# Optimization experiments

Hardware: AMD Instinct MI355X
Metric: run time of the kernel (lower is better)

The kernel has to match this reference:

```python
import jax, jax.numpy as jnp
import numpy as np

B, L, H, C = 32, 2048, 512, 50
KERNEL = 3  # avgpool kernel, stride 1, pad 1, count_include_pad=False


def _avgpool3_no_pad_count(x):
    """AvgPool1d(kernel=3, stride=1, pad=1, count_include_pad=False) along last axis.
    x: (..., L). Zero-pad, sum 3-tap windows, divide by number of valid elements."""
    pad = [(0, 0)] * (x.ndim - 1) + [(1, 1)]
    xp = jnp.pad(x, pad)
    s = xp[..., :-2] + xp[..., 1:-1] + xp[..., 2:]
    ones = jnp.pad(jnp.ones_like(x), pad)
    cnt = ones[..., :-2] + ones[..., 1:-1] + ones[..., 2:]
    return s / cnt


def setup_inputs() -> dict:
    key = jax.random.key(0)
    k1, k2, k3, k4, k5, k6 = jax.random.split(key, 6)
    sent_keys = jax.random.normal(k1, (B, L, H), dtype=jnp.float32)
    sent_values = jax.random.normal(k2, (B, L, H), dtype=jnp.float32)
    sent_lens = jax.random.randint(k3, (B,), 1, L + 1).astype(jnp.int64)
    W1 = jax.random.normal(k4, (H, H), dtype=jnp.float32) * 0.02
    W2 = jax.random.normal(k5, (H, H), dtype=jnp.float32) * 0.02
    W3 = jax.random.normal(k6, (C, H), dtype=jnp.float32) * 0.02
    return {"sent_keys": sent_keys, "sent_values": sent_values,
            "sent_lens": sent_lens, "W1": W1, "W2": W2, "W3": W3}


def reference(sent_keys, sent_values, sent_lens, W1, W2, W3):
    # Tiny MLP scorer (dropout is identity in eval mode)
    p1 = jnp.tanh(jnp.einsum('blh,kh->blk', sent_keys, W1))   # (B,L,H)
    p2 = jnp.tanh(jnp.einsum('blh,kh->blk', p1, W2))          # (B,L,H)
    p3 = jnp.einsum('blh,ch->blc', p1 + p2, W3)               # (B,L,C)

    b, l, c = p3.shape
    # Fill padded positions with the score at the last valid position (index len-1)
    last_idx = (sent_lens - 1).astype(jnp.int32)[:, None, None]        # (B,1,1)
    last = jnp.take_along_axis(p3, jnp.broadcast_to(last_idx, (b, 1, c)), axis=1)  # (B,1,C)
    mask = (jnp.arange(l)[None, :] < sent_lens[:, None])[:, :, None]   # (B,L,1)
    kq = jnp.where(mask, p3, last)

    # Smooth along doc-position axis with avgpool(count_include_pad=False)
    smoothened_kq = _avgpool3_no_pad_count(kq.transpose(0, 2, 1)).transpose(0, 2, 1)  # (B,L,C)

    # Softmax over classes, then zero out padded positions
    attention_values = jax.nn.softmax(smoothened_kq, axis=2)
    attention_values = jnp.where(mask, attention_values, 0.0)

    # (B,C,L) @ (B,L,H) -> (B,C,H)
    class_inputs = jnp.einsum('blc,blh->bch', attention_values, sent_values)
    return attention_values, class_inputs, smoothened_kq
```

## Files before the change

### kernel.cpp

```cpp
#include <hip/hip_runtime.h>
#include <cstdint>

#define Bc 32
#define Lc 2048
#define Hc 512
#define Cc 50
#define PCc 52
#define Mc (Bc*Lc)

typedef short s8v   __attribute__((ext_vector_type(8)));
typedef float f4v   __attribute__((ext_vector_type(4)));

__device__ inline unsigned short f2bf(float f) {
    unsigned int u = __float_as_uint(f);
    u += 0x7fffu + ((u >> 16) & 1u);
    return (unsigned short)(u >> 16);
}
__device__ inline float bf2f(unsigned short h) {
    return __uint_as_float(((unsigned int)h) << 16);
}
__device__ inline float fast_tanh(float x) {
    float e = __expf(2.0f * x);
    return 1.0f - 2.0f / (e + 1.0f);
}
__device__ inline void gl_lds16(const unsigned short* g, unsigned short* l) {
    __builtin_amdgcn_global_load_lds(
        (const __attribute__((address_space(1))) unsigned int*)g,
        (__attribute__((address_space(3))) unsigned int*)l, 16, 0, 0);
}

__global__ __launch_bounds__(256)
void f32_to_bf16_kernel(const float* __restrict__ in, unsigned short* __restrict__ out)
{
    size_t i = ((size_t)blockIdx.x * 256 + threadIdx.x) * 8;
    float4 a = *(const float4*)(in + i);
    float4 b = *(const float4*)(in + i + 4);
    s8v o;
    o[0]=f2bf(a.x); o[1]=f2bf(a.y); o[2]=f2bf(a.z); o[3]=f2bf(a.w);
    o[4]=f2bf(b.x); o[5]=f2bf(b.y); o[6]=f2bf(b.z); o[7]=f2bf(b.w);
    *(s8v*)(out + i) = o;
}

__global__ __launch_bounds__(256)
void convert_weights_kernel(const float* __restrict__ W1, const float* __restrict__ W2,
                            const float* __restrict__ W3,
                            unsigned short* __restrict__ W1b,
                            unsigned short* __restrict__ W2b,
                            unsigned short* __restrict__ W3b)
{
    int e = (blockIdx.x * 256 + threadIdx.x) * 8;
    if (e >= 524288) {
        int off = e - 524288;
        int row = off >> 9;
        s8v o;
        #pragma unroll
        for (int j = 0; j < 8; ++j)
            o[j] = (row < Cc) ? (short)f2bf(W3[off + j]) : (short)0;
        *(s8v*)(W3b + off) = o;
        return;
    }
    const float* src = (e < 262144) ? W1 : W2;
    unsigned short* dst = (e < 262144) ? W1b : W2b;
    int off = (e < 262144) ? e : e - 262144;
    float4 a = *(const float4*)(src + off);
    float4 b = *(const float4*)(src + off + 4);
    s8v o;
    o[0]=f2bf(a.x); o[1]=f2bf(a.y); o[2]=f2bf(a.z); o[3]=f2bf(a.w);
    o[4]=f2bf(b.x); o[5]=f2bf(b.y); o[6]=f2bf(b.z); o[7]=f2bf(b.w);
    *(s8v*)(dst + off) = o;
}

__global__ __launch_bounds__(256)
void transpose_v_kernel(const float* __restrict__ V, unsigned short* __restrict__ Vt)
{
    __shared__ float tile[64 * 65];
    const int l0 = blockIdx.x * 64;
    const int h0 = blockIdx.y * 64;
    const int b  = blockIdx.z;
    const int tid = threadIdx.x;
    const int li = tid >> 2;
    const int hq = (tid & 3) * 4;

    const float* src = V + ((size_t)(b * Lc + l0 + li)) * Hc + h0 + hq;
    #pragma unroll
    for (int j = 0; j < 4; ++j) {
        float4 v = *(const float4*)(src + 16 * j);
        float* d = &tile[li * 65 + hq + 16 * j];
        d[0] = v.x; d[1] = v.y; d[2] = v.z; d[3] = v.w;
    }
    __syncthreads();

    const int lane = tid & 63;
    const int w    = tid >> 6;
    #pragma unroll
    for (int i = 0; i < 16; ++i) {
        int hr = i * 4 + w;
        unsigned short* dst = Vt + ((size_t)(b * Hc + h0 + hr)) * Lc + l0 + lane;
        *dst = f2bf(tile[lane * 65 + hr]);
    }
}

__global__ __launch_bounds__(256)
void mfma_gemm512(const unsigned short* __restrict__ Ab,
                  const unsigned short* __restrict__ Wb,
                  unsigned short* __restrict__ Ob, int mode)
{
    __shared__ alignas(16) unsigned short As[128 * 32];
    __shared__ alignas(16) unsigned short Bs[128 * 32];
    const int tid = threadIdx.x;
    const int w = tid >> 6, l = tid & 63;
    const int j0 = blockIdx.x * 128;
    const int i0 = blockIdx.y * 128;

    const int sr  = w * 16 + (l >> 2);
    const int kg8 = (l & 3) * 8;
    const unsigned short* Ag0 = Ab + (size_t)(i0 + sr) * 512 + kg8;
    const unsigned short* Ag1 = Ag0 + (size_t)64 * 512;
    const unsigned short* Bg0 = Wb + (size_t)(j0 + sr) * 512 + kg8;
    const unsigned short* Bg1 = Bg0 + (size_t)64 * 512;
    unsigned short* Al0 = As + w * 512;
    unsigned short* Al1 = As + 2048 + w * 512;
    unsigned short* Bl0 = Bs + w * 512;
    unsigned short* Bl1 = Bs + 2048 + w * 512;

    const int wm = (w & 1) * 64, wn = (w >> 1) * 64;
    const int fr = l & 15;
    const int fq = (l >> 4) * 8;

    f4v acc[4][4];
    #pragma unroll
    for (int r = 0; r < 4; ++r)
        #pragma unroll
        for (int c = 0; c < 4; ++c) acc[r][c] = (f4v){0.f, 0.f, 0.f, 0.f};

    for (int k0 = 0; k0 < 512; k0 += 32) {
        gl_lds16(Ag0 + k0, Al0);
        gl_lds16(Ag1 + k0, Al1);
        gl_lds16(Bg0 + k0, Bl0);
        gl_lds16(Bg1 + k0, Bl1);
        __syncthreads();
        s8v af[4], bf[4];
        #pragma unroll
        for (int r = 0; r < 4; ++r)
            af[r] = *(const s8v*)&As[(wm + r * 16 + fr) * 32 + fq];
        #pragma unroll
        for (int c = 0; c < 4; ++c)
            bf[c] = *(const s8v*)&Bs[(wn + c * 16 + fr) * 32 + fq];
        #pragma unroll
        for (int r = 0; r < 4; ++r)
            #pragma unroll
            for (int c = 0; c < 4; ++c)
                acc[r][c] = __builtin_amdgcn_mfma_f32_16x16x32_bf16(
                    af[r], bf[c], acc[r][c], 0, 0, 0);
        __syncthreads();
    }

    #pragma unroll
    for (int r = 0; r < 4; ++r)
        #pragma unroll
        for (int v = 0; v < 4; ++v) {
            const int row = i0 + wm + r * 16 + (l >> 4) * 4 + v;
            #pragma unroll
            for (int c = 0; c < 4; ++c) {
                const int col = j0 + wn + c * 16 + fr;
                float x = fast_tanh(acc[r][c][v]);
                if (mode) x += bf2f(Ab[(size_t)row * 512 + col]);
                Ob[(size_t)row * 512 + col] = f2bf(x);
            }
        }
}

__global__ __launch_bounds__(256)
void mfma_gemm_p3(const unsigned short* __restrict__ Sb,
                  const unsigned short* __restrict__ W3b,
                  float* __restrict__ P3)
{
    __shared__ alignas(16) unsigned short As[128 * 32];
    __shared__ alignas(16) unsigned short Bs[64 * 32];
    const int tid = threadIdx.x;
    const int w = tid >> 6, l = tid & 63;
    const int i0 = blockIdx.x * 128;

    const int sr  = w * 16 + (l >> 2);
    const int kg8 = (l & 3) * 8;
    const unsigned short* Ag0 = Sb + (size_t)(i0 + sr) * 512 + kg8;
    const unsigned short* Ag1 = Ag0 + (size_t)64 * 512;
    const unsigned short* Bg  = W3b + (size_t)sr * 512 + kg8;
    unsigned short* Al0 = As + w * 512;
    unsigned short* Al1 = As + 2048 + w * 512;
    unsigned short* Bl  = Bs + w * 512;

    const int wm = w * 32;
    const int fr = l & 15;
    const int fq = (l >> 4) * 8;

    f4v acc[2][4];
    #pragma unroll
    for (int r = 0; r < 2; ++r)
        #pragma unroll
        for (int c = 0; c < 4; ++c) acc[r][c] = (f4v){0.f, 0.f, 0.f, 0.f};

    for (int k0 = 0; k0 < 512; k0 += 32) {
        gl_lds16(Ag0 + k0, Al0);
        gl_lds16(Ag1 + k0, Al1);
        gl_lds16(Bg + k0, Bl);
        __syncthreads();
        s8v af[2], bf[4];
        #pragma unroll
        for (int r = 0; r < 2; ++r)
            af[r] = *(const s8v*)&As[(wm + r * 16 + fr) * 32 + fq];
        #pragma unroll
        for (int c = 0; c < 4; ++c)
            bf[c] = *(const s8v*)&Bs[(c * 16 + fr) * 32 + fq];
        #pragma unroll
        for (int r = 0; r < 2; ++r)
            #pragma unroll
            for (int c = 0; c < 4; ++c)
                acc[r][c] = __builtin_amdgcn_mfma_f32_16x16x32_bf16(
                    af[r], bf[c], acc[r][c], 0, 0, 0);
        __syncthreads();
    }

    #pragma unroll
    for (int r = 0; r < 2; ++r)
        #pragma unroll
        for (int v = 0; v < 4; ++v) {
            const int row = i0 + wm + r * 16 + (l >> 4) * 4 + v;
            #pragma unroll
            for (int c = 0; c < 4; ++c) {
                const int col = c * 16 + fr;
                if (col < Cc) P3[(size_t)row * PCc + col] = acc[r][c][v];
            }
        }
}

__global__ __launch_bounds__(64)
void normalize_lens_kernel(const int* __restrict__ raw, int* __restrict__ lens)
{
    __shared__ int is64;
    if (threadIdx.x == 0) {
        int orv = 0;
        for (int i = 1; i < 32; i += 2) orv |= raw[i];
        is64 = (orv == 0) ? 1 : 0;
    }
    __syncthreads();
    int b = threadIdx.x;
    if (b < Bc) lens[b] = is64 ? raw[2*b] : raw[b];
}

__global__ __launch_bounds__(256)
void pool_softmax_kernel(const float* __restrict__ P3, const int* __restrict__ lens,
                         float* __restrict__ out_attn, float* __restrict__ out_smooth,
                         unsigned short* __restrict__ attnT)
{
    const int idx = blockIdx.x * 256 + threadIdx.x;
    const int b = idx >> 11;
    const int l = idx & (Lc - 1);
    const int len = lens[b];
    const float* base = P3 + (size_t)b * Lc * PCc;

    const int  r0 = min(l, len - 1);
    const bool hm = (l > 0);
    const bool hp = (l < Lc - 1);
    const int  rm = hm ? min(l - 1, len - 1) : 0;
    const int  rp = hp ? min(l + 1, len - 1) : 0;
    const float rcnt = 1.f / (1.f + (hm ? 1.f : 0.f) + (hp ? 1.f : 0.f));

    float sm[PCc];
    const float* p0 = base + (size_t)r0 * PCc;
    #pragma unroll
    for (int q = 0; q < 13; ++q) {
        f4v v = *(const f4v*)(p0 + q * 4);
        sm[q*4+0] = v[0]; sm[q*4+1] = v[1]; sm[q*4+2] = v[2]; sm[q*4+3] = v[3];
    }
    if (hm) {
        const float* p = base + (size_t)rm * PCc;
        #pragma unroll
        for (int q = 0; q < 13; ++q) {
            f4v v = *(const f4v*)(p + q * 4);
            sm[q*4+0] += v[0]; sm[q*4+1] += v[1]; sm[q*4+2] += v[2]; sm[q*4+3] += v[3];
        }
    }
    if (hp) {
        const float* p = base + (size_t)rp * PCc;
        #pragma unroll
        for (int q = 0; q < 13; ++q) {
            f4v v = *(const f4v*)(p + q * 4);
            sm[q*4+0] += v[0]; sm[q*4+1] += v[1]; sm[q*4+2] += v[2]; sm[q*4+3] += v[3];
        }
    }

    float mx = -1e30f;
    #pragma unroll
    for (int c = 0; c < Cc; ++c) {
        sm[c] *= rcnt;
        mx = fmaxf(mx, sm[c]);
    }
    float* srow = out_smooth + (size_t)idx * Cc;
    #pragma unroll
    for (int q = 0; q < 25; ++q) {
        float2 v = make_float2(sm[q*2], sm[q*2+1]);
        *(float2*)(srow + q * 2) = v;
    }

    float sum = 0.f;
    #pragma unroll
    for (int c = 0; c < Cc; ++c) {
        float e = __expf(sm[c] - mx);
        sm[c] = e;
        sum += e;
    }
    const float inv = 1.f / sum;
    const bool valid = (l < len);
    const float scale = valid ? inv : 0.f;
    float* arow = out_attn + (size_t)idx * Cc;
    unsigned short* trow = attnT + (size_t)b * 64 * Lc + l;
    #pragma unroll
    for (int c = 0; c < Cc; ++c) sm[c] *= scale;
    #pragma unroll
    for (int q = 0; q < 25; ++q)
        *(float2*)(arow + q * 2) = make_float2(sm[q*2], sm[q*2+1]);
    #pragma unroll
    for (int c = 0; c < Cc; ++c)
        trow[(size_t)c * Lc] = f2bf(sm[c]);
}

__global__ __launch_bounds__(256)
void class_mfma_kernel(const unsigned short* __restrict__ attnT,
                       const unsigned short* __restrict__ Vt,
                       float* __restrict__ out_class)
{
    __shared__ alignas(16) unsigned short As[64 * 32];
    __shared__ alignas(16) unsigned short Bs[128 * 32];
    const int tid = threadIdx.x;
    const int w = tid >> 6, l = tid & 63;
    const int n0 = blockIdx.x * 128;
    const int b  = blockIdx.y;
    const int kb = blockIdx.z * 512;

    const int sr  = w * 16 + (l >> 2);
    const int kg8 = (l & 3) * 8;
    const unsigned short* Ag  = attnT + ((size_t)b * 64 + sr) * Lc + kg8;
    const unsigned short* Bg0 = Vt + ((size_t)(b * Hc + n0 + sr)) * Lc + kg8;
    const unsigned short* Bg1 = Bg0 + (size_t)64 * Lc;
    unsigned short* Al  = As + w * 512;
    unsigned short* Bl0 = Bs + w * 512;
    unsigned short* Bl1 = Bs + 2048 + w * 512;

    const int fr = l & 15;
    const int fq = (l >> 4) * 8;

    f4v acc[4][2];
    #pragma unroll
    for (int r = 0; r < 4; ++r)
        #pragma unroll
        for (int c = 0; c < 2; ++c) acc[r][c] = (f4v){0.f, 0.f, 0.f, 0.f};

    for (int k0 = kb; k0 < kb + 512; k0 += 32) {
        gl_lds16(Ag + k0, Al);
        gl_lds16(Bg0 + k0, Bl0);
        gl_lds16(Bg1 + k0, Bl1);
        __syncthreads();
        s8v af[4], bf[2];
        #pragma unroll
        for (int r = 0; r < 4; ++r)
            af[r] = *(const s8v*)&As[(r * 16 + fr) * 32 + fq];
        #pragma unroll
        for (int c = 0; c < 2; ++c)
            bf[c] = *(const s8v*)&Bs[(w * 32 + c * 16 + fr) * 32 + fq];
        #pragma unroll
        for (int r = 0; r < 4; ++r)
            #pragma unroll
            for (int c = 0; c < 2; ++c)
                acc[r][c] = __builtin_amdgcn_mfma_f32_16x16x32_bf16(
                    af[r], bf[c], acc[r][c], 0, 0, 0);
        __syncthreads();
    }

    #pragma unroll
    for (int r = 0; r < 4; ++r)
        #pragma unroll
        for (int v = 0; v < 4; ++v) {
            const int m = r * 16 + (l >> 4) * 4 + v;
            if (m < Cc) {
                #pragma unroll
                for (int c = 0; c < 2; ++c) {
                    const int h = n0 + w * 32 + c * 16 + fr;
                    atomicAdd(out_class + ((size_t)b * Cc + m) * Hc + h,
                              acc[r][c][v]);
                }
            }
        }
}

extern "C" void kernel_launch(void* const* d_in, const int* in_sizes, int n_in,
                              void* d_out, int out_size, void* d_ws, size_t ws_size,
                              hipStream_t stream)
{
    const float* keys     = (const float*)d_in[0];
    const float* vals     = (const float*)d_in[1];
    const int*   lens_raw = (const int*)d_in[2];
    const float* W1       = (const float*)d_in[3];
    const float* W2       = (const float*)d_in[4];
    const float* W3       = (const float*)d_in[5];

    char* ws = (char*)d_ws;
    const size_t MB = 1024 * 1024;
    unsigned short* Akv  = (unsigned short*)ws;
    float*          P3   = (float*)ws;
    unsigned short* P1b  = (unsigned short*)(ws + 64 * MB);
    unsigned short* Vt   = (unsigned short*)(ws + 64 * MB);
    unsigned short* Sb   = (unsigned short*)(ws + 128 * MB);
    unsigned short* W1b  = (unsigned short*)(ws + 192 * MB);
    unsigned short* W2b  = W1b + Hc * Hc;
    unsigned short* W3b  = W2b + Hc * Hc;
    unsigned short* attnT= (unsigned short*)(ws + 194 * MB);
    int*            lens = (int*)(ws + 202 * MB);

    float* out_attn   = (float*)d_out;
    float* out_class  = out_attn + (size_t)Bc * Lc * Cc;
    float* out_smooth = out_class + (size_t)Bc * Cc * Hc;

    hipMemsetAsync(out_class, 0, (size_t)Bc * Cc * Hc * sizeof(float), stream);

    f32_to_bf16_kernel<<<(Mc * Hc / 8) / 256, 256, 0, stream>>>(keys, Akv);
    convert_weights_kernel<<<272, 256, 0, stream>>>(W1, W2, W3, W1b, W2b, W3b);
    normalize_lens_kernel<<<1, 64, 0, stream>>>(lens_raw, lens);

    mfma_gemm512<<<dim3(4, Mc / 128), 256, 0, stream>>>(Akv, W1b, P1b, 0);
    mfma_gemm512<<<dim3(4, Mc / 128), 256, 0, stream>>>(P1b, W2b, Sb, 1);
    transpose_v_kernel<<<dim3(Lc / 64, Hc / 64, Bc), 256, 0, stream>>>(vals, Vt);
    mfma_gemm_p3<<<Mc / 128, 256, 0, stream>>>(Sb, W3b, P3);
    pool_softmax_kernel<<<Mc / 256, 256, 0, stream>>>(P3, lens, out_attn, out_smooth, attnT);
    class_mfma_kernel<<<dim3(4, Bc, 4), 256, 0, stream>>>(attnT, Vt, out_class);
}
```

Baseline: 523.4 us.

## Stage GEMM epilogue through LDS for coalesced bf16 stores and remap blocks for XCD locality

The 512x512 GEMM epilogue now writes tanh results into a padded shared-memory tile in four 32-row passes, then reads them back so each thread stores (and for mode 1, loads the residual) four contiguous bf16 values. This replaces scattered 2-byte global stores and loads. The launch becomes a 1D grid with a block-index remap so that blocks on the same XCD (bid mod 8) work on nearby row tiles and share the A rows. In exchange it adds about 17KB of LDS per block and extra barriers, which may reduce occupancy.

```diff
diff --git a/kernel.cpp b/kernel.cpp
--- a/kernel.cpp
+++ b/kernel.cpp
@@ -107,10 +107,16 @@
 {
     __shared__ alignas(16) unsigned short As[128 * 32];
     __shared__ alignas(16) unsigned short Bs[128 * 32];
+    __shared__ alignas(16) float Esf[32 * 133];
     const int tid = threadIdx.x;
     const int w = tid >> 6, l = tid & 63;
-    const int j0 = blockIdx.x * 128;
-    const int i0 = blockIdx.y * 128;
+
+    const int bid = blockIdx.x;
+    const int ixd = bid >> 3;
+    const int y   = (bid & 7) * 64 + (ixd >> 2);
+    const int x   = ixd & 3;
+    const int j0 = x * 128;
+    const int i0 = y * 128;
 
     const int sr  = w * 16 + (l >> 2);
     const int kg8 = (l & 3) * 8;
@@ -156,18 +162,44 @@
     }
 
     #pragma unroll
-    for (int r = 0; r < 4; ++r)
-        #pragma unroll
-        for (int v = 0; v < 4; ++v) {
-            const int row = i0 + wm + r * 16 + (l >> 4) * 4 + v;
+    for (int h = 0; h < 4; ++h) {
+        if (h) __syncthreads();
+        if ((w & 1) == (h >> 1)) {
+            const int rr = (h & 1) * 2;
             #pragma unroll
-            for (int c = 0; c < 4; ++c) {
-                const int col = j0 + wn + c * 16 + fr;
-                float x = fast_tanh(acc[r][c][v]);
-                if (mode) x += bf2f(Ab[(size_t)row * 512 + col]);
-                Ob[(size_t)row * 512 + col] = f2bf(x);
+            for (int r = 0; r < 2; ++r)
+                #pragma unroll
+                for (int c = 0; c < 4; ++c)
+                    #pragma unroll
+                    for (int v = 0; v < 4; ++v) {
+                        int row = r * 16 + (l >> 4) * 4 + v;
+                        int col = wn + c * 16 + fr;
+                        Esf[row * 133 + col] = fast_tanh(acc[rr + r][c][v]);
+                    }
+        }
+        __syncthreads();
+        #pragma unroll
+        for (int t = 0; t < 4; ++t) {
+            int chunk = t * 256 + tid;
+            int row = chunk >> 5;
+            int c4  = (chunk & 31) * 4;
+            f4v val = *(const f4v*)&Esf[row * 133 + c4];
+            size_t gr   = (size_t)(i0 + (h >> 1) * 64 + (h & 1) * 32 + row);
+            size_t goff = gr * 512 + j0 + c4;
+            ushort4 o;
+            if (mode) {
+                ushort4 a = *(const ushort4*)(Ab + goff);
+                o.x = f2bf(val[0] + bf2f(a.x));
+                o.y = f2bf(val[1] + bf2f(a.y));
+                o.z = f2bf(val[2] + bf2f(a.z));
+                o.w = f2bf(val[3] + bf2f(a.w));
+            } else {
+                o.x = f2bf(val[0]); o.y = f2bf(val[1]);
+                o.z = f2bf(val[2]); o.w = f2bf(val[3]);
             }
-        }
+            *(ushort4*)(Ob + goff) = o;
+        }
+    }
 }
 
 __global__ __launch_bounds__(256)
@@ -427,8 +459,8 @@
     convert_weights_kernel<<<272, 256, 0, stream>>>(W1, W2, W3, W1b, W2b, W3b);
     normalize_lens_kernel<<<1, 64, 0, stream>>>(lens_raw, lens);
 
-    mfma_gemm512<<<dim3(4, Mc / 128), 256, 0, stream>>>(Akv, W1b, P1b, 0);
-    mfma_gemm512<<<dim3(4, Mc / 128), 256, 0, stream>>>(P1b, W2b, Sb, 1);
+    mfma_gemm512<<<2048, 256, 0, stream>>>(Akv, W1b, P1b, 0);
+    mfma_gemm512<<<2048, 256, 0, stream>>>(P1b, W2b, Sb, 1);
     transpose_v_kernel<<<dim3(Lc / 64, Hc / 64, Bc), 256, 0, stream>>>(vals, Vt);
     mfma_gemm_p3<<<Mc / 128, 256, 0, stream>>>(Sb, W3b, P3);
     pool_softmax_kernel<<<Mc / 256, 256, 0, stream>>>(P3, lens, out_attn, out_smooth, attnT);
```

After: 499.0 us. 4.7% less time.
